# Performance work log

Hardware: AMD Instinct MI355X
Metric: run time of the kernel (lower is better)

Reference implementation:

```python
import jax, jax.numpy as jnp
import numpy as np
import math

B, S, D, H = 4, 2048, 1024, 16
DH = D // H  # head dim = 64


def setup_inputs() -> dict:
    key = jax.random.key(0)
    ks = jax.random.split(key, 6)
    x = jax.random.normal(ks[0], (B, S, D), dtype=jnp.float32)
    mask = jax.random.randint(ks[1], (B, 1, S, S), 0, 2, dtype=jnp.int32)
    # torch nn.Linear default init scale ~ 1/sqrt(fan_in); use small scale for stability
    w_qkv = jax.random.normal(ks[2], (D, 3 * D), dtype=jnp.float32) * (1.0 / math.sqrt(D))
    b_qkv = jax.random.normal(ks[3], (3 * D,), dtype=jnp.float32) * 0.01
    w_out = jax.random.normal(ks[4], (D, D), dtype=jnp.float32) * (1.0 / math.sqrt(D))
    b_out = jax.random.normal(ks[5], (D,), dtype=jnp.float32) * 0.01
    return {"x": x, "mask": mask, "w_qkv": w_qkv, "b_qkv": b_qkv, "w_out": w_out, "b_out": b_out}


def reference(x, mask, w_qkv, b_qkv, w_out, b_out):
    # Fused QKV projection: [B,S,3D]
    qkv = x @ w_qkv + b_qkv
    q, k, v = qkv[..., :D], qkv[..., D:2 * D], qkv[..., 2 * D:]
    # split heads -> [B,H,S,DH]
    def split(t):
        return t.reshape(B, S, H, DH).transpose(0, 2, 1, 3)
    q, k, v = split(q), split(k), split(v)
    # scores: [B,H,S,S]
    scores = jnp.einsum("bhqd,bhkd->bhqk", q, k) / jnp.sqrt(jnp.float32(DH))
    scores = jnp.where(mask == 0, jnp.float32(-1000.0), scores)
    attn = jax.nn.softmax(scores, axis=-1)
    ctx = jnp.einsum("bhqk,bhkd->bhqd", attn, v)  # [B,H,S,DH]
    ctx = ctx.transpose(0, 2, 1, 3).reshape(B, S, D)
    return ctx @ w_out + b_out
```

## Files before the change

### kernel.cpp

```cpp
#include <hip/hip_runtime.h>
#include <hip/hip_bf16.h>
#include <stdint.h>

#define B_  4
#define S_  2048
#define D_  1024
#define H_  16
#define DH_ 64
#define N3_ 3072

typedef __attribute__((ext_vector_type(8))) short  short8;
typedef __attribute__((ext_vector_type(8))) unsigned short ushort8;
typedef __attribute__((ext_vector_type(4))) float  float4v;

__device__ __forceinline__ float bf2f(unsigned short u) {
    union { unsigned int i; float f; } c; c.i = ((unsigned int)u) << 16; return c.f;
}
__device__ __forceinline__ unsigned short f2bf(float f) {
    union { float f; unsigned int i; } c; c.f = f;
    unsigned int x = c.i;
    return (unsigned short)((x + 0x7FFFu + ((x >> 16) & 1u)) >> 16);
}
__device__ __forceinline__ unsigned short f2bf_hu(float f) {
    union { float f; unsigned int i; } c; c.f = f;
    return (unsigned short)((c.i + 0x8000u) >> 16);
}

__device__ __forceinline__ void gll16(const void* g, void* l) {
    __builtin_amdgcn_global_load_lds(
        (const __attribute__((address_space(1))) unsigned int*)g,
        (__attribute__((address_space(3))) unsigned int*)l, 16, 0, 0);
}

__global__ __launch_bounds__(256) void convert_x(
    const float* __restrict__ in, unsigned short* __restrict__ out, int n8)
{
    int g = blockIdx.x * 256 + threadIdx.x;
    if (g >= n8) return;
    const float4* p = (const float4*)(in + (size_t)g * 8);
    float4 a = p[0], b = p[1];
    ushort8 o;
    o[0] = f2bf(a.x); o[1] = f2bf(a.y); o[2] = f2bf(a.z); o[3] = f2bf(a.w);
    o[4] = f2bf(b.x); o[5] = f2bf(b.y); o[6] = f2bf(b.z); o[7] = f2bf(b.w);
    *(ushort8*)(out + (size_t)g * 8) = o;
}

__global__ __launch_bounds__(256) void convert_wT(
    const float* __restrict__ w, unsigned short* __restrict__ wt, int K, int N)
{
    __shared__ float t[32][33];
    const int row = threadIdx.x >> 5;
    const int col = threadIdx.x & 31;
    const int n0 = blockIdx.x * 32;
    const int k0 = blockIdx.y * 32;
#pragma unroll
    for (int i = 0; i < 4; ++i)
        t[row + 8 * i][col] = w[(size_t)(k0 + row + 8 * i) * N + n0 + col];
    __syncthreads();
#pragma unroll
    for (int i = 0; i < 4; ++i)
        wt[(size_t)(n0 + row + 8 * i) * K + k0 + col] = f2bf(t[col][row + 8 * i]);
}

template <int MODE>
__global__ __launch_bounds__(256) void gemm_bt(
    const unsigned short* __restrict__ a, const unsigned short* __restrict__ bt,
    const float* __restrict__ bias,
    unsigned short* __restrict__ q, unsigned short* __restrict__ k,
    unsigned short* __restrict__ v, float* __restrict__ out,
    int K, int N)
{
    __shared__ unsigned short As[128][64];
    __shared__ unsigned short Bs[128][64];

    const int tid  = threadIdx.x;
    const int wave = tid >> 6;
    const int lane = tid & 63;
    const int col  = lane & 15;
    const int quad = lane >> 4;
    const int wm   = (wave & 1) * 64;
    const int wn   = (wave >> 1) * 64;

    const int m0 = blockIdx.y * 128;
    const int n0 = blockIdx.x * 128;

    const int srow0 = wave * 32 + (lane >> 3);
    const int scg   = (lane & 7) ^ (lane >> 3);

    float4v acc[4][4] = {};

    for (int kt = 0; kt < K; kt += 64) {
#pragma unroll
        for (int c = 0; c < 4; ++c) {
            int row = srow0 + c * 8;
            gll16(a  + (size_t)(m0 + row) * K + kt + scg * 8,
                  (char*)As + wave * 4096 + c * 1024);
            gll16(bt + (size_t)(n0 + row) * K + kt + scg * 8,
                  (char*)Bs + wave * 4096 + c * 1024);
        }
        __syncthreads();

#pragma unroll
        for (int ks = 0; ks < 64; ks += 32) {
            const int sa = (((ks >> 3) + quad) ^ (col & 7)) * 8;
            short8 af[4], bf[4];
#pragma unroll
            for (int mi = 0; mi < 4; ++mi)
                af[mi] = *(const short8*)&As[wm + mi * 16 + col][sa];
#pragma unroll
            for (int ni = 0; ni < 4; ++ni)
                bf[ni] = *(const short8*)&Bs[wn + ni * 16 + col][sa];
#pragma unroll
            for (int mi = 0; mi < 4; ++mi)
#pragma unroll
                for (int ni = 0; ni < 4; ++ni)
                    acc[mi][ni] = __builtin_amdgcn_mfma_f32_16x16x32_bf16(
                        af[mi], bf[ni], acc[mi][ni], 0, 0, 0);
        }
        __syncthreads();
    }

#pragma unroll
    for (int mi = 0; mi < 4; ++mi) {
#pragma unroll
        for (int ni = 0; ni < 4; ++ni) {
            int n = n0 + wn + ni * 16 + col;
            float bv = bias[n];
#pragma unroll
            for (int r = 0; r < 4; ++r) {
                int m = m0 + wm + mi * 16 + quad * 4 + r;
                float val = acc[mi][ni][r] + bv;
                if (MODE == 0) {
                    int which = n >> 10;
                    int h  = (n & 1023) >> 6;
                    int dh = n & 63;
                    int bb = m >> 11;
                    int s  = m & 2047;
                    size_t off;
                    if (which == 2)
                        off = (((size_t)bb * H_ + h) * DH_ + dh) * S_ + s;
                    else
                        off = (((size_t)bb * H_ + h) * S_ + s) * DH_ + dh;
                    unsigned short* dst = (which == 0) ? q : ((which == 1) ? k : v);
                    dst[off] = f2bf(val);
                } else {
                    out[(size_t)m * N + n] = val;
                }
            }
        }
    }
}

__global__ __launch_bounds__(256) void attn_mfma(
    const unsigned short* __restrict__ q, const unsigned short* __restrict__ k,
    const unsigned short* __restrict__ vT, const int* __restrict__ mask,
    unsigned short* __restrict__ ctx)
{
    __shared__ unsigned short Ks[64][64];
    __shared__ unsigned short Vt[64][64];
    __shared__ unsigned short Ps[4][16][64];

    const int tid  = threadIdx.x;
    const int wave = tid >> 6;
    const int lane = tid & 63;
    const int col  = lane & 15;
    const int quad = lane >> 4;

    const int h  = blockIdx.y;
    const int bb = blockIdx.z;
    const int q0 = blockIdx.x * 64 + wave * 16;
    const int kvbase = ((bb * H_ + h) * S_) * DH_;
    const int vtbase = ((bb * H_ + h) * DH_) * S_;

    const float SC = 0.18033688011112042f;
    const unsigned short* qrow = q + kvbase + (q0 + col) * DH_;
    ushort8 qr0 = *(const ushort8*)(qrow + quad * 8);
    ushort8 qr1 = *(const ushort8*)(qrow + 32 + quad * 8);
    short8 qa0, qa1;
#pragma unroll
    for (int j = 0; j < 8; ++j) {
        qa0[j] = (short)f2bf(bf2f(qr0[j]) * SC);
        qa1[j] = (short)f2bf(bf2f(qr1[j]) * SC);
    }
    const float MASKED = -1442.6951f;

    const int* mptr[4];
#pragma unroll
    for (int r = 0; r < 4; ++r)
        mptr[r] = mask + (bb * S_ + q0 + quad * 4 + r) * S_ + col;

    const int sw2   = wave & 1;
    const int srow0 = sw2 * 32 + (lane >> 3);
    const int scg   = (lane & 7) ^ (lane >> 3);
    const int sw0   = (quad ^ (col & 7)) * 8;
    const int sw1   = ((4 + quad) ^ (col & 7)) * 8;

    float4v oacc[4] = {};
    float rsum[4] = {0.f, 0.f, 0.f, 0.f};

    for (int kt = 0; kt < S_ / 64; ++kt) {
        const int key0 = kt * 64;

        int mk[4][4];
#pragma unroll
        for (int sub = 0; sub < 4; ++sub)
#pragma unroll
            for (int r = 0; r < 4; ++r)
                mk[sub][r] = mptr[r][key0 + sub * 16];

#pragma unroll
        for (int c = 0; c < 4; ++c) {
            int r = srow0 + c * 8;
            if (wave < 2)
                gll16(k + kvbase + (key0 + r) * DH_ + scg * 8,
                      (char*)Ks + sw2 * 4096 + c * 1024);
            else
                gll16(vT + vtbase + r * S_ + key0 + scg * 8,
                      (char*)Vt + sw2 * 4096 + c * 1024);
        }
        __syncthreads();

        float4v sc[4];
#pragma unroll
        for (int sub = 0; sub < 4; ++sub) {
            short8 b0 = *(const short8*)&Ks[sub * 16 + col][sw0];
            short8 b1 = *(const short8*)&Ks[sub * 16 + col][sw1];
            float4v acs = {};
            acs = __builtin_amdgcn_mfma_f32_16x16x32_bf16(qa0, b0, acs, 0, 0, 0);
            acs = __builtin_amdgcn_mfma_f32_16x16x32_bf16(qa1, b1, acs, 0, 0, 0);
            sc[sub] = acs;
        }

#pragma unroll
        for (int sub = 0; sub < 4; ++sub)
#pragma unroll
        for (int r = 0; r < 4; ++r) {
            float s = (mk[sub][r] == 0) ? MASKED : sc[sub][r];
            float p = __builtin_amdgcn_exp2f(s);
            rsum[r] += p;
            int rowp = quad * 4 + r;
            int sg = (sub * 2 + (col >> 3)) ^ (rowp & 7);
            Ps[wave][rowp][sg * 8 + (col & 7)] = f2bf_hu(p);
        }

        short8 pa0 = *(const short8*)&Ps[wave][col][sw0];
        short8 pa1 = *(const short8*)&Ps[wave][col][sw1];
#pragma unroll
        for (int n = 0; n < 4; ++n) {
            short8 vb0 = *(const short8*)&Vt[n * 16 + col][sw0];
            short8 vb1 = *(const short8*)&Vt[n * 16 + col][sw1];
            oacc[n] = __builtin_amdgcn_mfma_f32_16x16x32_bf16(pa0, vb0, oacc[n], 0, 0, 0);
            oacc[n] = __builtin_amdgcn_mfma_f32_16x16x32_bf16(pa1, vb1, oacc[n], 0, 0, 0);
        }
        __syncthreads();
    }

    float inv[4];
#pragma unroll
    for (int r = 0; r < 4; ++r) {
        float s = rsum[r];
#pragma unroll
        for (int msk = 1; msk < 16; msk <<= 1)
            s += __shfl_xor(s, msk);
        inv[r] = 1.0f / s;
    }
#pragma unroll
    for (int n = 0; n < 4; ++n)
#pragma unroll
    for (int r = 0; r < 4; ++r) {
        size_t off = ((size_t)bb * S_ + (q0 + quad * 4 + r)) * D_
                   + h * DH_ + n * 16 + col;
        ctx[off] = f2bf(oacc[n][r] * inv[r]);
    }
}

extern "C" void kernel_launch(void* const* d_in, const int* in_sizes, int n_in,
                              void* d_out, int out_size, void* d_ws, size_t ws_size,
                              hipStream_t stream)
{
    const float* x     = (const float*)d_in[0];
    const int*   mask  = (const int*)d_in[1];
    const float* w_qkv = (const float*)d_in[2];
    const float* b_qkv = (const float*)d_in[3];
    const float* w_out = (const float*)d_in[4];
    const float* b_out = (const float*)d_in[5];
    float* out = (float*)d_out;

    unsigned short* ws = (unsigned short*)d_ws;
    const size_t sz = (size_t)B_ * S_ * D_;
    unsigned short* q     = ws;
    unsigned short* kk    = ws + sz;
    unsigned short* v     = ws + 2 * sz;
    unsigned short* ctx   = ws + 3 * sz;
    unsigned short* xbf   = ws + 4 * sz;
    unsigned short* wqkvT = ws + 5 * sz;
    unsigned short* woutT = ws + 5 * sz + (size_t)N3_ * D_;

    convert_x<<<(int)(sz / (256 * 8)), 256, 0, stream>>>(x, xbf, (int)(sz / 8));
    convert_wT<<<dim3(N3_ / 32, D_ / 32), 256, 0, stream>>>(w_qkv, wqkvT, D_, N3_);
    convert_wT<<<dim3(D_ / 32, D_ / 32), 256, 0, stream>>>(w_out, woutT, D_, D_);

    gemm_bt<0><<<dim3(N3_ / 128, (B_ * S_) / 128), 256, 0, stream>>>(
        xbf, wqkvT, b_qkv, q, kk, v, nullptr, D_, N3_);

    attn_mfma<<<dim3(S_ / 64, H_, B_), 256, 0, stream>>>(q, kk, v, mask, ctx);

    gemm_bt<1><<<dim3(D_ / 128, (B_ * S_) / 128), 256, 0, stream>>>(
        ctx, woutT, b_out, nullptr, nullptr, nullptr, out, D_, D_);
}
```

Baseline: 381.0 us.

## Double-buffer K/V tiles and transpose score MFMA for vectorized mask loads

Adds a second LDS buffer for K and V so the async load of the next 64-key tile overlaps compute on the current one, with the loop unrolled by two. The QK MFMA operands are swapped so each lane holds scores for one query row, which lets the mask be read as contiguous int4 loads. P is then written to LDS as packed 64-bit stores, and the row sums reduce with fewer shuffles. This costs extra LDS and register pressure from two in-flight mask sets, which may lower occupancy.

```diff
diff --git a/kernel.cpp b/kernel.cpp
--- a/kernel.cpp
+++ b/kernel.cpp
@@ -156,8 +156,8 @@
     const unsigned short* __restrict__ vT, const int* __restrict__ mask,
     unsigned short* __restrict__ ctx)
 {
-    __shared__ unsigned short Ks[64][64];
-    __shared__ unsigned short Vt[64][64];
+    __shared__ unsigned short Ks[2][64][64];
+    __shared__ unsigned short Vt[2][64][64];
     __shared__ unsigned short Ps[4][16][64];
 
     const int tid  = threadIdx.x;
@@ -184,10 +184,7 @@
     }
     const float MASKED = -1442.6951f;
 
-    const int* mptr[4];
-#pragma unroll
-    for (int r = 0; r < 4; ++r)
-        mptr[r] = mask + (bb * S_ + q0 + quad * 4 + r) * S_ + col;
+    const int* mrow = mask + ((size_t)bb * S_ + q0 + col) * S_ + quad * 4;
 
     const int sw2   = wave & 1;
     const int srow0 = sw2 * 32 + (lane >> 3);
@@ -196,81 +193,100 @@
     const int sw1   = ((4 + quad) ^ (col & 7)) * 8;
 
     float4v oacc[4] = {};
-    float rsum[4] = {0.f, 0.f, 0.f, 0.f};
-
-    for (int kt = 0; kt < S_ / 64; ++kt) {
+    float rsum = 0.f;
+
+    auto STAGE = [&](int buf, int kt) {
         const int key0 = kt * 64;
-
-        int mk[4][4];
-#pragma unroll
-        for (int sub = 0; sub < 4; ++sub)
-#pragma unroll
-            for (int r = 0; r < 4; ++r)
-                mk[sub][r] = mptr[r][key0 + sub * 16];
-
 #pragma unroll
         for (int c = 0; c < 4; ++c) {
             int r = srow0 + c * 8;
             if (wave < 2)
                 gll16(k + kvbase + (key0 + r) * DH_ + scg * 8,
-                      (char*)Ks + sw2 * 4096 + c * 1024);
+                      (char*)Ks + buf * 8192 + sw2 * 4096 + c * 1024);
             else
                 gll16(vT + vtbase + r * S_ + key0 + scg * 8,
-                      (char*)Vt + sw2 * 4096 + c * 1024);
-        }
-        __syncthreads();
-
+                      (char*)Vt + buf * 8192 + sw2 * 4096 + c * 1024);
+        }
+    };
+
+    auto LOADMASK = [&](int4 (&m)[4], int kt) {
+        const int* p = mrow + kt * 64;
+#pragma unroll
+        for (int sub = 0; sub < 4; ++sub)
+            m[sub] = *(const int4*)(p + sub * 16);
+    };
+
+    auto TILE = [&](int buf, const int4 (&mu)[4]) {
         float4v sc[4];
 #pragma unroll
         for (int sub = 0; sub < 4; ++sub) {
-            short8 b0 = *(const short8*)&Ks[sub * 16 + col][sw0];
-            short8 b1 = *(const short8*)&Ks[sub * 16 + col][sw1];
+            short8 a0 = *(const short8*)&Ks[buf][sub * 16 + col][sw0];
+            short8 a1 = *(const short8*)&Ks[buf][sub * 16 + col][sw1];
             float4v acs = {};
-            acs = __builtin_amdgcn_mfma_f32_16x16x32_bf16(qa0, b0, acs, 0, 0, 0);
-            acs = __builtin_amdgcn_mfma_f32_16x16x32_bf16(qa1, b1, acs, 0, 0, 0);
+            acs = __builtin_amdgcn_mfma_f32_16x16x32_bf16(a0, qa0, acs, 0, 0, 0);
+            acs = __builtin_amdgcn_mfma_f32_16x16x32_bf16(a1, qa1, acs, 0, 0, 0);
             sc[sub] = acs;
         }
-
-#pragma unroll
-        for (int sub = 0; sub < 4; ++sub)
-#pragma unroll
-        for (int r = 0; r < 4; ++r) {
-            float s = (mk[sub][r] == 0) ? MASKED : sc[sub][r];
-            float p = __builtin_amdgcn_exp2f(s);
-            rsum[r] += p;
-            int rowp = quad * 4 + r;
-            int sg = (sub * 2 + (col >> 3)) ^ (rowp & 7);
-            Ps[wave][rowp][sg * 8 + (col & 7)] = f2bf_hu(p);
-        }
-
+#pragma unroll
+        for (int sub = 0; sub < 4; ++sub) {
+            int mm[4] = { mu[sub].x, mu[sub].y, mu[sub].z, mu[sub].w };
+            float p[4];
+#pragma unroll
+            for (int r = 0; r < 4; ++r) {
+                float s = (mm[r] == 0) ? MASKED : sc[sub][r];
+                p[r] = __builtin_amdgcn_exp2f(s);
+                rsum += p[r];
+            }
+            unsigned int u0 = ((unsigned int)f2bf_hu(p[1]) << 16) | f2bf_hu(p[0]);
+            unsigned int u1 = ((unsigned int)f2bf_hu(p[3]) << 16) | f2bf_hu(p[2]);
+            int sg = (2 * sub + (quad >> 1)) ^ (col & 7);
+            uint2 w; w.x = u0; w.y = u1;
+            *(uint2*)((char*)&Ps[wave][0][0] + col * 128 + sg * 16 + (quad & 1) * 8) = w;
+        }
         short8 pa0 = *(const short8*)&Ps[wave][col][sw0];
         short8 pa1 = *(const short8*)&Ps[wave][col][sw1];
 #pragma unroll
         for (int n = 0; n < 4; ++n) {
-            short8 vb0 = *(const short8*)&Vt[n * 16 + col][sw0];
-            short8 vb1 = *(const short8*)&Vt[n * 16 + col][sw1];
+            short8 vb0 = *(const short8*)&Vt[buf][n * 16 + col][sw0];
+            short8 vb1 = *(const short8*)&Vt[buf][n * 16 + col][sw1];
             oacc[n] = __builtin_amdgcn_mfma_f32_16x16x32_bf16(pa0, vb0, oacc[n], 0, 0, 0);
             oacc[n] = __builtin_amdgcn_mfma_f32_16x16x32_bf16(pa1, vb1, oacc[n], 0, 0, 0);
         }
+    };
+
+    int4 mA[4], mB[4];
+    LOADMASK(mA, 0);
+    STAGE(0, 0);
+#pragma unroll 1
+    for (int kt2 = 0; kt2 < S_ / 128; ++kt2) {
+        const int ke = kt2 * 2, ko = ke + 1;
         __syncthreads();
-    }
-
-    float inv[4];
-#pragma unroll
-    for (int r = 0; r < 4; ++r) {
-        float s = rsum[r];
-#pragma unroll
-        for (int msk = 1; msk < 16; msk <<= 1)
-            s += __shfl_xor(s, msk);
-        inv[r] = 1.0f / s;
-    }
+        LOADMASK(mB, ko);
+        STAGE(1, ko);
+        TILE(0, mA);
+        __syncthreads();
+        if (kt2 < S_ / 128 - 1) {
+            LOADMASK(mA, ke + 2);
+            STAGE(0, ke + 2);
+        }
+        TILE(1, mB);
+    }
+
+    float s = rsum;
+    s += __shfl_xor(s, 16);
+    s += __shfl_xor(s, 32);
+    float invs = 1.0f / s;
+    float inv4[4];
+#pragma unroll
+    for (int r = 0; r < 4; ++r)
+        inv4[r] = __shfl(invs, quad * 20 + r);
 #pragma unroll
     for (int n = 0; n < 4; ++n)
 #pragma unroll
     for (int r = 0; r < 4; ++r) {
         size_t off = ((size_t)bb * S_ + (q0 + quad * 4 + r)) * D_
                    + h * DH_ + n * 16 + col;
-        ctx[off] = f2bf(oacc[n][r] * inv[r]);
+        ctx[off] = f2bf(oacc[n][r] * inv4[r]);
     }
 }
 
```

Measured after the change: 421.9 us. 10.7% more time.

## Process two 64-query blocks per attention workgroup to reuse K/V tiles

Applied to the files above, without the earlier changes.

Each attention block now covers 128 queries instead of 64: every wave handles two 16-row query slices and shares each loaded K and V^T tile between them. This halves the number of workgroups and the global K/V traffic per query, and gives more MFMA work per barrier. The cost is doubled accumulator registers (launch_bounds raised to request 4 waves/SIMD occupancy hint), a larger P scratch buffer, and fewer blocks (1024) to fill the GPU.

```diff
diff --git a/kernel.cpp b/kernel.cpp
--- a/kernel.cpp
+++ b/kernel.cpp
@@ -151,14 +151,14 @@
     }
 }
 
-__global__ __launch_bounds__(256) void attn_mfma(
+__global__ __launch_bounds__(256, 4) void attn_mfma(
     const unsigned short* __restrict__ q, const unsigned short* __restrict__ k,
     const unsigned short* __restrict__ vT, const int* __restrict__ mask,
     unsigned short* __restrict__ ctx)
 {
     __shared__ unsigned short Ks[64][64];
     __shared__ unsigned short Vt[64][64];
-    __shared__ unsigned short Ps[4][16][64];
+    __shared__ unsigned short Ps[4][2][16][64];
 
     const int tid  = threadIdx.x;
     const int wave = tid >> 6;
@@ -168,26 +168,30 @@
 
     const int h  = blockIdx.y;
     const int bb = blockIdx.z;
-    const int q0 = blockIdx.x * 64 + wave * 16;
+    const int q0 = blockIdx.x * 128 + wave * 16;
     const int kvbase = ((bb * H_ + h) * S_) * DH_;
     const int vtbase = ((bb * H_ + h) * DH_) * S_;
 
     const float SC = 0.18033688011112042f;
-    const unsigned short* qrow = q + kvbase + (q0 + col) * DH_;
-    ushort8 qr0 = *(const ushort8*)(qrow + quad * 8);
-    ushort8 qr1 = *(const ushort8*)(qrow + 32 + quad * 8);
-    short8 qa0, qa1;
-#pragma unroll
-    for (int j = 0; j < 8; ++j) {
-        qa0[j] = (short)f2bf(bf2f(qr0[j]) * SC);
-        qa1[j] = (short)f2bf(bf2f(qr1[j]) * SC);
+    short8 qa[2][2];
+#pragma unroll
+    for (int qb = 0; qb < 2; ++qb) {
+        const unsigned short* qrow = q + kvbase + (q0 + qb * 64 + col) * DH_;
+        ushort8 qr0 = *(const ushort8*)(qrow + quad * 8);
+        ushort8 qr1 = *(const ushort8*)(qrow + 32 + quad * 8);
+#pragma unroll
+        for (int j = 0; j < 8; ++j) {
+            qa[qb][0][j] = (short)f2bf(bf2f(qr0[j]) * SC);
+            qa[qb][1][j] = (short)f2bf(bf2f(qr1[j]) * SC);
+        }
     }
     const float MASKED = -1442.6951f;
 
     const int* mptr[4];
 #pragma unroll
     for (int r = 0; r < 4; ++r)
-        mptr[r] = mask + (bb * S_ + q0 + quad * 4 + r) * S_ + col;
+        mptr[r] = mask + ((size_t)bb * S_ + q0 + quad * 4 + r) * S_ + col;
+    const int QB1 = 64 * S_;
 
     const int sw2   = wave & 1;
     const int srow0 = sw2 * 32 + (lane >> 3);
@@ -195,18 +199,19 @@
     const int sw0   = (quad ^ (col & 7)) * 8;
     const int sw1   = ((4 + quad) ^ (col & 7)) * 8;
 
-    float4v oacc[4] = {};
-    float rsum[4] = {0.f, 0.f, 0.f, 0.f};
+    float4v oaccA[4] = {}, oaccB[4] = {};
+    float rsumA[4] = {0.f, 0.f, 0.f, 0.f};
+    float rsumB[4] = {0.f, 0.f, 0.f, 0.f};
 
     for (int kt = 0; kt < S_ / 64; ++kt) {
         const int key0 = kt * 64;
 
-        int mk[4][4];
+        int mk0[4][4];
 #pragma unroll
         for (int sub = 0; sub < 4; ++sub)
 #pragma unroll
             for (int r = 0; r < 4; ++r)
-                mk[sub][r] = mptr[r][key0 + sub * 16];
+                mk0[sub][r] = mptr[r][key0 + sub * 16];
 
 #pragma unroll
         for (int c = 0; c < 4; ++c) {
@@ -220,57 +225,88 @@
         }
         __syncthreads();
 
-        float4v sc[4];
+        float4v scA[4], scB[4];
 #pragma unroll
         for (int sub = 0; sub < 4; ++sub) {
             short8 b0 = *(const short8*)&Ks[sub * 16 + col][sw0];
             short8 b1 = *(const short8*)&Ks[sub * 16 + col][sw1];
-            float4v acs = {};
-            acs = __builtin_amdgcn_mfma_f32_16x16x32_bf16(qa0, b0, acs, 0, 0, 0);
-            acs = __builtin_amdgcn_mfma_f32_16x16x32_bf16(qa1, b1, acs, 0, 0, 0);
-            sc[sub] = acs;
-        }
-
+            float4v t0 = {}, t1 = {};
+            t0 = __builtin_amdgcn_mfma_f32_16x16x32_bf16(qa[0][0], b0, t0, 0, 0, 0);
+            t0 = __builtin_amdgcn_mfma_f32_16x16x32_bf16(qa[0][1], b1, t0, 0, 0, 0);
+            t1 = __builtin_amdgcn_mfma_f32_16x16x32_bf16(qa[1][0], b0, t1, 0, 0, 0);
+            t1 = __builtin_amdgcn_mfma_f32_16x16x32_bf16(qa[1][1], b1, t1, 0, 0, 0);
+            scA[sub] = t0; scB[sub] = t1;
+        }
+
+        int mk1[4][4];
 #pragma unroll
         for (int sub = 0; sub < 4; ++sub)
 #pragma unroll
+            for (int r = 0; r < 4; ++r)
+                mk1[sub][r] = mptr[r][QB1 + key0 + sub * 16];
+
+#pragma unroll
+        for (int sub = 0; sub < 4; ++sub)
+#pragma unroll
         for (int r = 0; r < 4; ++r) {
-            float s = (mk[sub][r] == 0) ? MASKED : sc[sub][r];
+            float s = (mk0[sub][r] == 0) ? MASKED : scA[sub][r];
             float p = __builtin_amdgcn_exp2f(s);
-            rsum[r] += p;
+            rsumA[r] += p;
             int rowp = quad * 4 + r;
             int sg = (sub * 2 + (col >> 3)) ^ (rowp & 7);
-            Ps[wave][rowp][sg * 8 + (col & 7)] = f2bf_hu(p);
-        }
-
-        short8 pa0 = *(const short8*)&Ps[wave][col][sw0];
-        short8 pa1 = *(const short8*)&Ps[wave][col][sw1];
+            Ps[wave][0][rowp][sg * 8 + (col & 7)] = f2bf_hu(p);
+        }
+#pragma unroll
+        for (int sub = 0; sub < 4; ++sub)
+#pragma unroll
+        for (int r = 0; r < 4; ++r) {
+            float s = (mk1[sub][r] == 0) ? MASKED : scB[sub][r];
+            float p = __builtin_amdgcn_exp2f(s);
+            rsumB[r] += p;
+            int rowp = quad * 4 + r;
+            int sg = (sub * 2 + (col >> 3)) ^ (rowp & 7);
+            Ps[wave][1][rowp][sg * 8 + (col & 7)] = f2bf_hu(p);
+        }
+
+        short8 paA0 = *(const short8*)&Ps[wave][0][col][sw0];
+        short8 paA1 = *(const short8*)&Ps[wave][0][col][sw1];
+        short8 paB0 = *(const short8*)&Ps[wave][1][col][sw0];
+        short8 paB1 = *(const short8*)&Ps[wave][1][col][sw1];
+
 #pragma unroll
         for (int n = 0; n < 4; ++n) {
             short8 vb0 = *(const short8*)&Vt[n * 16 + col][sw0];
             short8 vb1 = *(const short8*)&Vt[n * 16 + col][sw1];
-            oacc[n] = __builtin_amdgcn_mfma_f32_16x16x32_bf16(pa0, vb0, oacc[n], 0, 0, 0);
-            oacc[n] = __builtin_amdgcn_mfma_f32_16x16x32_bf16(pa1, vb1, oacc[n], 0, 0, 0);
+            oaccA[n] = __builtin_amdgcn_mfma_f32_16x16x32_bf16(paA0, vb0, oaccA[n], 0, 0, 0);
+            oaccA[n] = __builtin_amdgcn_mfma_f32_16x16x32_bf16(paA1, vb1, oaccA[n], 0, 0, 0);
+            oaccB[n] = __builtin_amdgcn_mfma_f32_16x16x32_bf16(paB0, vb0, oaccB[n], 0, 0, 0);
+            oaccB[n] = __builtin_amdgcn_mfma_f32_16x16x32_bf16(paB1, vb1, oaccB[n], 0, 0, 0);
         }
         __syncthreads();
     }
 
-    float inv[4];
+    float invA[4], invB[4];
 #pragma unroll
     for (int r = 0; r < 4; ++r) {
-        float s = rsum[r];
-#pragma unroll
-        for (int msk = 1; msk < 16; msk <<= 1)
-            s += __shfl_xor(s, msk);
-        inv[r] = 1.0f / s;
+        float sA = rsumA[r], sB = rsumB[r];
+#pragma unroll
+        for (int msk = 1; msk < 16; msk <<= 1) {
+            sA += __shfl_xor(sA, msk);
+            sB += __shfl_xor(sB, msk);
+        }
+        invA[r] = 1.0f / sA;
+        invB[r] = 1.0f / sB;
     }
 #pragma unroll
     for (int n = 0; n < 4; ++n)
 #pragma unroll
     for (int r = 0; r < 4; ++r) {
-        size_t off = ((size_t)bb * S_ + (q0 + quad * 4 + r)) * D_
-                   + h * DH_ + n * 16 + col;
-        ctx[off] = f2bf(oacc[n][r] * inv[r]);
+        size_t offA = ((size_t)bb * S_ + (q0 + quad * 4 + r)) * D_
+                    + h * DH_ + n * 16 + col;
+        ctx[offA] = f2bf(oaccA[n][r] * invA[r]);
+        size_t offB = ((size_t)bb * S_ + (q0 + 64 + quad * 4 + r)) * D_
+                    + h * DH_ + n * 16 + col;
+        ctx[offB] = f2bf(oaccB[n][r] * invB[r]);
     }
 }
 
@@ -303,7 +339,7 @@
     gemm_bt<0><<<dim3(N3_ / 128, (B_ * S_) / 128), 256, 0, stream>>>(
         xbf, wqkvT, b_qkv, q, kk, v, nullptr, D_, N3_);
 
-    attn_mfma<<<dim3(S_ / 64, H_, B_), 256, 0, stream>>>(q, kk, v, mask, ctx);
+    attn_mfma<<<dim3(S_ / 128, H_, B_), 256, 0, stream>>>(q, kk, v, mask, ctx);
 
     gemm_bt<1><<<dim3(D_ / 128, (B_ * S_) / 128), 256, 0, stream>>>(
         ctx, woutT, b_out, nullptr, nullptr, nullptr, out, D_, D_);
```

After: 608.1 us. 59.6% more time.
